# Kernel optimization log

Hardware: AMD Instinct MI355X
Metric: run time of the kernel (lower is better)

## Reference

```python
import jax, jax.numpy as jnp
import numpy as np

N_NODES = 100_000
N_EDGES = 1_250_000
N_GRAPHS = 2048


def gcn_conv(x, src, dst, norm, W, b, n):
    # PyG GCNConv: x' = D^-1/2 (A+I) D^-1/2 (x W) + b  (self-loops already in src/dst)
    h = x @ W                                   # [N, 64]
    msg = h[src] * norm[:, None]                # [E+N, 64] gather + scale
    out = jax.ops.segment_sum(msg, dst, num_segments=n)  # scatter-add
    return out + b


def build_norm(edge_index, n):
    # add self loops, compute symmetric gcn normalization
    loop = jnp.arange(n, dtype=edge_index.dtype)
    src = jnp.concatenate([edge_index[0], loop])
    dst = jnp.concatenate([edge_index[1], loop])
    deg = jax.ops.segment_sum(jnp.ones_like(dst, dtype=jnp.float32), dst, num_segments=n)
    dinv = jnp.where(deg > 0, jax.lax.rsqrt(deg), 0.0)
    norm = dinv[src] * dinv[dst]
    return src, dst, norm


def setup_inputs() -> dict:
    key = jax.random.key(0)
    ks = jax.random.split(key, 11)
    return {
        "x": jax.random.randint(ks[0], (N_NODES,), 0, 28, dtype=jnp.int32),
        "edge_index": jax.random.randint(ks[1], (2, N_EDGES), 0, N_NODES, dtype=jnp.int32),
        "edge_attr": jax.random.randint(ks[2], (N_EDGES,), 0, 4, dtype=jnp.int32),
        "batch": jnp.sort(jax.random.randint(ks[3], (N_NODES,), 0, N_GRAPHS, dtype=jnp.int32)),
        "emb_table": jax.random.normal(ks[4], (28, 64), dtype=jnp.float32),
        "W1": jax.random.normal(ks[5], (64, 64), dtype=jnp.float32) * 0.125,
        "b1": jax.random.normal(ks[6], (64,), dtype=jnp.float32) * 0.02,
        "W2": jax.random.normal(ks[7], (64, 64), dtype=jnp.float32) * 0.125,
        "b2": jax.random.normal(ks[8], (64,), dtype=jnp.float32) * 0.02,
        "lin_W": jax.random.normal(ks[9], (64, 1), dtype=jnp.float32) * 0.125,
        "lin_b": jax.random.normal(ks[10], (1,), dtype=jnp.float32) * 0.02,
    }


def reference(x, edge_index, edge_attr, batch, emb_table, W1, b1, W2, b2, lin_W, lin_b):
    n = x.shape[0]
    src, dst, norm = build_norm(edge_index, n)
    h = emb_table[x]                                   # node embedding lookup [N, 64]
    h = jax.nn.relu(gcn_conv(h, src, dst, norm, W1, b1, n))
    # dropout is identity at inference (training=False)
    emb = gcn_conv(h, src, dst, norm, W2, b2, n)        # [N, 64]
    y = emb @ lin_W + lin_b                              # [N, 1]
    out = jax.ops.segment_sum(y, batch, num_segments=N_GRAPHS)  # graph readout
    return out.squeeze(-1)                               # [N_GRAPHS]
```

## Files before the change

### kernel.cpp

```cpp
#include <hip/hip_runtime.h>

#define N_CLS 28
#define DIM   64
#define VB    128
#define VB_SH 7
#define SLK   32
#define NBKT_S 800
#define PT_T  512
#define IPT   12
#define PTILE (PT_T * IPT)
#define STG   9280

__global__ void __launch_bounds__(PT_T)
k_part(const int* __restrict__ src, const int* __restrict__ dst,
       int* __restrict__ ebkt,
       const float* __restrict__ emb, const float* __restrict__ W1,
       const float* __restrict__ W2, const float* __restrict__ linW,
       const float* __restrict__ b2, const float* __restrict__ linb,
       float* __restrict__ T1g, float* __restrict__ ug, float* __restrict__ ccg,
       float* __restrict__ out,
       int E, int nbkt, int nblk, int out_size) {
    int tid = threadIdx.x, b = blockIdx.x;
    if (b == nblk) {
        int lane = tid & 63, wv = tid >> 6;
        for (int r = wv; r < N_CLS; r += PT_T / 64) {
            float acc = 0.f;
#pragma unroll
            for (int k = 0; k < DIM; ++k) acc += emb[r * DIM + k] * W1[k * DIM + lane];
            T1g[r * DIM + lane] = acc;
        }
        if (wv == 0) {
            float acc = 0.f;
#pragma unroll
            for (int k = 0; k < DIM; ++k) acc += W2[lane * DIM + k] * linW[k];
            ug[lane] = acc;
        }
        if (tid == 0) {
            float s = 0.f;
            for (int k = 0; k < DIM; ++k) s += b2[k] * linW[k];
            ccg[0] = s + linb[0];
        }
        for (int i = tid; i < out_size; i += PT_T) out[i] = 0.f;
        return;
    }
    __shared__ int h[NBKT_S];
    __shared__ int offs[NBKT_S];
    __shared__ int sc[1024];
    __shared__ __align__(16) int stage[STG];
    for (int i = tid; i < nbkt; i += PT_T) h[i] = 0;
    __syncthreads();
    int s0 = b * PTILE;
    int pk[IPT], ar[IPT];
#pragma unroll
    for (int g = 0; g < IPT / 4; ++g) {
        int i4 = s0 + (g * PT_T + tid) * 4;
        if (i4 + 3 < E) {
            int4 sv = *(const int4*)&src[i4];
            int4 dv = *(const int4*)&dst[i4];
            int ss[4] = {sv.x, sv.y, sv.z, sv.w};
            int dd[4] = {dv.x, dv.y, dv.z, dv.w};
#pragma unroll
            for (int j = 0; j < 4; ++j) {
                int bkt = dd[j] >> VB_SH;
                int r = atomicAdd(&h[bkt], 1);
                pk[g * 4 + j] = ss[j] | ((dd[j] & (VB - 1)) << 17);
                ar[g * 4 + j] = bkt | (r << 10);
            }
        } else {
#pragma unroll
            for (int j = 0; j < 4; ++j) {
                int idx = i4 + j;
                ar[g * 4 + j] = -1;
                if (idx < E) {
                    int s = src[idx], d = dst[idx];
                    int bkt = d >> VB_SH;
                    int r = atomicAdd(&h[bkt], 1);
                    pk[g * 4 + j] = s | ((d & (VB - 1)) << 17);
                    ar[g * 4 + j] = bkt | (r << 10);
                }
            }
        }
    }
    __syncthreads();
    int w0 = (tid < nbkt) ? ((min(h[tid], SLK - 1) + 4) & ~3) : 0;
    int w1 = (tid + 512 < nbkt) ? ((min(h[tid + 512], SLK - 1) + 4) & ~3) : 0;
    sc[tid] = w0; sc[tid + 512] = w1;
    __syncthreads();
    for (int o = 1; o < 1024; o <<= 1) {
        int a0 = (tid >= o) ? sc[tid - o] : 0;
        int a1 = (tid + 512 >= o) ? sc[tid + 512 - o] : 0;
        __syncthreads();
        sc[tid] += a0; sc[tid + 512] += a1;
        __syncthreads();
    }
    if (tid < nbkt) offs[tid] = sc[tid] - w0;
    if (tid + 512 < nbkt) offs[tid + 512] = sc[tid + 512] - w1;
    __syncthreads();
    for (int i = tid; i < nbkt; i += PT_T) stage[offs[i]] = min(h[i], SLK - 1);
#pragma unroll
    for (int k = 0; k < IPT; ++k) {
        int a = ar[k];
        if (a >= 0) {
            int bkt = a & 1023, r = a >> 10;
            if (r < SLK - 1) stage[offs[bkt] + 1 + r] = pk[k];
        }
    }
    __syncthreads();
    for (int i = tid; i < nbkt; i += PT_T) {
        int c = min(h[i], SLK - 1);
        int nq = (c + 4) >> 2;
        int4* gq = (int4*)(ebkt + ((size_t)i * nblk + b) * SLK);
        const int4* sq = (const int4*)&stage[offs[i]];
        for (int q = 0; q < nq; ++q) gq[q] = sq[q];
    }
}

#define RUN_FOREACH(rv, BODY)                                            \
    {                                                                    \
        int4 q0 = (rv)[0];                                               \
        int c = q0.x;                                                    \
        int e3[3] = {q0.y, q0.z, q0.w};                                  \
        _Pragma("unroll")                                                \
        for (int j = 0; j < 3; ++j) if (j < c) { int p = e3[j]; BODY; }  \
        for (int base = 3; base < c; base += 4) {                        \
            int4 q = (rv)[(base + 1) >> 2];                              \
            int e4[4] = {q.x, q.y, q.z, q.w};                            \
            _Pragma("unroll")                                            \
            for (int j = 0; j < 4; ++j)                                  \
                if (base + j < c) { int p = e4[j]; BODY; }               \
        }                                                                \
    }

__global__ void __launch_bounds__(256)
k_deg(const int* __restrict__ ebkt, const int* __restrict__ x,
      float2* __restrict__ xd, int N, int nblk) {
    __shared__ int dg[VB];
    int tid = threadIdx.x, k = blockIdx.x;
    if (tid < VB) dg[tid] = 0;
    __syncthreads();
    if (tid < nblk) {
        const int4* rv = (const int4*)(ebkt + ((size_t)k * nblk + tid) * SLK);
        RUN_FOREACH(rv, atomicAdd(&dg[p >> 17], 1));
    }
    __syncthreads();
    int v = k * VB + tid;
    if (tid < VB && v < N)
        xd[v] = make_float2(rsqrtf((float)(dg[tid] + 1)), __int_as_float(x[v]));
}

__global__ void __launch_bounds__(256)
k_l1(const int* __restrict__ ebkt, const float2* __restrict__ xd,
     const float* __restrict__ T1, const float* __restrict__ b1,
     const float* __restrict__ u, float* __restrict__ t, int N, int nblk) {
    __shared__ __align__(16) float cnt[VB * N_CLS];
    __shared__ float T1s[N_CLS * DIM];
    __shared__ float b1s[DIM], us[DIM];
    int tid = threadIdx.x, b = blockIdx.x;
    for (int i = tid; i < VB * N_CLS; i += 256) cnt[i] = 0.f;
    for (int i = tid; i < N_CLS * DIM; i += 256) T1s[i] = T1[i];
    if (tid < DIM) { b1s[tid] = b1[tid]; us[tid] = u[tid]; }
    __syncthreads();
    if (tid < nblk) {
        const int4* rv = (const int4*)(ebkt + ((size_t)b * nblk + tid) * SLK);
        RUN_FOREACH(rv, {
            float2 xs = xd[p & 0x1FFFF];
            atomicAdd(&cnt[(p >> 17) * N_CLS + __float_as_int(xs.y)], xs.x);
        });
    }
    __syncthreads();
    int wave = tid >> 6, lane = tid & 63;
    float tc[N_CLS];
#pragma unroll
    for (int c = 0; c < N_CLS; ++c) tc[c] = T1s[c * DIM + lane];
    int v0 = b * VB;
#pragma unroll 4
    for (int it = 0; it < VB / 4; ++it) {
        int lv = wave * (VB / 4) + it;
        int v = v0 + lv;
        if (v >= N) break;
        float2 pv = xd[v];
        float dv = pv.x;
        int xv = __float_as_int(pv.y);
        const float4* row = (const float4*)&cnt[lv * N_CLS];
        float acc = dv * T1s[xv * DIM + lane];
#pragma unroll
        for (int q4 = 0; q4 < 7; ++q4) {
            float4 r = row[q4];
            acc += r.x * tc[q4 * 4 + 0] + r.y * tc[q4 * 4 + 1]
                 + r.z * tc[q4 * 4 + 2] + r.w * tc[q4 * 4 + 3];
        }
        float hh = fmaxf(dv * acc + b1s[lane], 0.f);
        float q = hh * us[lane];
#pragma unroll
        for (int off = 32; off; off >>= 1) q += __shfl_down(q, off);
        if (lane == 0) t[v] = dv * q;
    }
}

__global__ void __launch_bounds__(256)
k_l2(const int* __restrict__ ebkt, const float2* __restrict__ xd,
     const float* __restrict__ t, const float* __restrict__ cc,
     const int* __restrict__ batch, float* __restrict__ out,
     int N, int n_graphs, int nblk) {
    __shared__ float acc[VB];
    __shared__ float og[64];
    __shared__ int g0s;
    int tid = threadIdx.x, k = blockIdx.x;
    if (tid < VB) acc[tid] = 0.f;
    if (tid < 64) og[tid] = 0.f;
    if (tid == 0) g0s = batch[min(k * VB, N - 1)];
    __syncthreads();
    if (tid < nblk) {
        const int4* rv = (const int4*)(ebkt + ((size_t)k * nblk + tid) * SLK);
        RUN_FOREACH(rv, atomicAdd(&acc[p >> 17], t[p & 0x1FFFF]));
    }
    __syncthreads();
    int v = k * VB + tid;
    if (tid < VB && v < N) {
        float y = xd[v].x * (acc[tid] + t[v]) + cc[0];
        int g = batch[v];
        int off = g - g0s;
        if (off < 64) atomicAdd(&og[off], y);
        else atomicAdd(&out[g], y);
    }
    __syncthreads();
    if (tid < 64) {
        float val = og[tid];
        int g = g0s + tid;
        if (val != 0.f && g < n_graphs) atomicAdd(&out[g], val);
    }
}

extern "C" void kernel_launch(void* const* d_in, const int* in_sizes, int n_in,
                              void* d_out, int out_size, void* d_ws, size_t ws_size,
                              hipStream_t stream) {
    const int*   x     = (const int*)d_in[0];
    const int*   ei    = (const int*)d_in[1];
    const int*   batch = (const int*)d_in[3];
    const float* emb   = (const float*)d_in[4];
    const float* W1    = (const float*)d_in[5];
    const float* b1    = (const float*)d_in[6];
    const float* W2    = (const float*)d_in[7];
    const float* b2    = (const float*)d_in[8];
    const float* linW  = (const float*)d_in[9];
    const float* linb  = (const float*)d_in[10];

    const int N = in_sizes[0];
    const int E = in_sizes[1] / 2;
    const int* srcp = ei;
    const int* dstp = ei + E;
    float* out = (float*)d_out;

    const int nbkt = (N + VB - 1) >> VB_SH;
    const int nblk = (E + PTILE - 1) / PTILE;

    char* w = (char*)d_ws;
    float2* xd   = (float2*)w; w += (size_t)N * 8;
    float*  t    = (float*)w;  w += (size_t)N * 4;
    int*    ebkt = (int*)w;    w += (size_t)nbkt * nblk * SLK * 4;
    float*  T1   = (float*)w;  w += (size_t)N_CLS * DIM * 4;
    float*  u    = (float*)w;  w += DIM * 4;
    float*  cc   = (float*)w;  w += 16;

    k_part<<<nblk + 1, PT_T, 0, stream>>>(srcp, dstp, ebkt,
                                          emb, W1, W2, linW, b2, linb,
                                          T1, u, cc, out, E, nbkt, nblk, out_size);
    k_deg <<<nbkt, 256, 0, stream>>>(ebkt, x, xd, N, nblk);
    k_l1  <<<nbkt, 256, 0, stream>>>(ebkt, xd, T1, b1, u, t, N, nblk);
    k_l2  <<<nbkt, 256, 0, stream>>>(ebkt, xd, t, cc, batch, out, N, out_size, nblk);
}
```

Before: 70.55 us.

## Split bucket runs across thread pairs, use wave-level scans and DPP reductions

The three consumer kernels now launch 512 threads per block, and each run of bucketed edges is processed by two threads that take alternating elements, halving the serial per-thread chain. The partition kernel replaces its 1024-element block-wide Hillis-Steele scan in shared memory with shuffle-based wave scans plus a small per-wave total array, which cuts down on barriers. In k_l1 the 64-lane reduction uses DPP row operations instead of shuffles, and the result is written from lane 63. The extra threads raise register and occupancy pressure in k_l1, and both threads of a pair still read the same run data.

```diff
diff --git a/kernel.cpp b/kernel.cpp
--- a/kernel.cpp
+++ b/kernel.cpp
@@ -45,7 +45,8 @@
     }
     __shared__ int h[NBKT_S];
     __shared__ int offs[NBKT_S];
-    __shared__ int sc[1024];
+    __shared__ int wt[8];
+    __shared__ int seg0tot;
     __shared__ __align__(16) int stage[STG];
     for (int i = tid; i < nbkt; i += PT_T) h[i] = 0;
     __syncthreads();
@@ -82,20 +83,41 @@
         }
     }
     __syncthreads();
-    int w0 = (tid < nbkt) ? ((min(h[tid], SLK - 1) + 4) & ~3) : 0;
-    int w1 = (tid + 512 < nbkt) ? ((min(h[tid + 512], SLK - 1) + 4) & ~3) : 0;
-    sc[tid] = w0; sc[tid + 512] = w1;
-    __syncthreads();
-    for (int o = 1; o < 1024; o <<= 1) {
-        int a0 = (tid >= o) ? sc[tid - o] : 0;
-        int a1 = (tid + 512 >= o) ? sc[tid + 512 - o] : 0;
+    int lane = tid & 63, wave = tid >> 6;
+    {
+        int w0 = (tid < nbkt) ? ((min(h[tid], SLK - 1) + 4) & ~3) : 0;
+        int incl = w0;
+#pragma unroll
+        for (int o = 1; o < 64; o <<= 1) {
+            int n = __shfl_up(incl, o);
+            if (lane >= o) incl += n;
+        }
+        if (lane == 63) wt[wave] = incl;
         __syncthreads();
-        sc[tid] += a0; sc[tid + 512] += a1;
+        int woff = 0, tot = 0;
+#pragma unroll
+        for (int w2 = 0; w2 < 8; ++w2) { int t2 = wt[w2]; woff += (w2 < wave) ? t2 : 0; tot += t2; }
+        if (tid < nbkt) offs[tid] = woff + incl - w0;
+        if (tid == 0) seg0tot = tot;
         __syncthreads();
     }
-    if (tid < nbkt) offs[tid] = sc[tid] - w0;
-    if (tid + 512 < nbkt) offs[tid + 512] = sc[tid + 512] - w1;
-    __syncthreads();
+    {
+        int i1 = tid + 512;
+        int w1 = (i1 < nbkt) ? ((min(h[i1], SLK - 1) + 4) & ~3) : 0;
+        int incl = w1;
+#pragma unroll
+        for (int o = 1; o < 64; o <<= 1) {
+            int n = __shfl_up(incl, o);
+            if (lane >= o) incl += n;
+        }
+        if (lane == 63) wt[wave] = incl;
+        __syncthreads();
+        int woff = 0;
+#pragma unroll
+        for (int w2 = 0; w2 < 8; ++w2) woff += (w2 < wave) ? wt[w2] : 0;
+        if (i1 < nbkt) offs[i1] = seg0tot + woff + incl - w1;
+        __syncthreads();
+    }
     for (int i = tid; i < nbkt; i += PT_T) stage[offs[i]] = min(h[i], SLK - 1);
 #pragma unroll
     for (int k = 0; k < IPT; ++k) {
@@ -115,32 +137,45 @@
     }
 }
 
-#define RUN_FOREACH(rv, BODY)                                            \
+#define RUN_FOREACH_J(rv, jj, BODY)                                      \
     {                                                                    \
         int4 q0 = (rv)[0];                                               \
         int c = q0.x;                                                    \
         int e3[3] = {q0.y, q0.z, q0.w};                                  \
         _Pragma("unroll")                                                \
-        for (int j = 0; j < 3; ++j) if (j < c) { int p = e3[j]; BODY; }  \
+        for (int j_ = 0; j_ < 3; ++j_)                                   \
+            if (j_ < c && (j_ & 1) == (jj)) { int p = e3[j_]; BODY; }    \
         for (int base = 3; base < c; base += 4) {                        \
             int4 q = (rv)[(base + 1) >> 2];                              \
             int e4[4] = {q.x, q.y, q.z, q.w};                            \
             _Pragma("unroll")                                            \
-            for (int j = 0; j < 4; ++j)                                  \
-                if (base + j < c) { int p = e4[j]; BODY; }               \
+            for (int j_ = 0; j_ < 4; ++j_)                               \
+                if (base + j_ < c && ((base + j_) & 1) == (jj))          \
+                    { int p = e4[j_]; BODY; }                            \
         }                                                                \
     }
 
-__global__ void __launch_bounds__(256)
+__device__ __forceinline__ float wsum64(float q) {
+    q += __int_as_float(__builtin_amdgcn_update_dpp(0, __float_as_int(q), 0x111, 0xf, 0xf, true));
+    q += __int_as_float(__builtin_amdgcn_update_dpp(0, __float_as_int(q), 0x112, 0xf, 0xf, true));
+    q += __int_as_float(__builtin_amdgcn_update_dpp(0, __float_as_int(q), 0x114, 0xf, 0xf, true));
+    q += __int_as_float(__builtin_amdgcn_update_dpp(0, __float_as_int(q), 0x118, 0xf, 0xf, true));
+    q += __int_as_float(__builtin_amdgcn_update_dpp(0, __float_as_int(q), 0x142, 0xa, 0xf, false));
+    q += __int_as_float(__builtin_amdgcn_update_dpp(0, __float_as_int(q), 0x143, 0xc, 0xf, false));
+    return q;
+}
+
+__global__ void __launch_bounds__(512)
 k_deg(const int* __restrict__ ebkt, const int* __restrict__ x,
       float2* __restrict__ xd, int N, int nblk) {
     __shared__ int dg[VB];
     int tid = threadIdx.x, k = blockIdx.x;
     if (tid < VB) dg[tid] = 0;
     __syncthreads();
-    if (tid < nblk) {
-        const int4* rv = (const int4*)(ebkt + ((size_t)k * nblk + tid) * SLK);
-        RUN_FOREACH(rv, atomicAdd(&dg[p >> 17], 1));
+    int rid = tid >> 1, j = tid & 1;
+    if (rid < nblk) {
+        const int4* rv = (const int4*)(ebkt + ((size_t)k * nblk + rid) * SLK);
+        RUN_FOREACH_J(rv, j, atomicAdd(&dg[p >> 17], 1));
     }
     __syncthreads();
     int v = k * VB + tid;
@@ -148,7 +183,7 @@
         xd[v] = make_float2(rsqrtf((float)(dg[tid] + 1)), __int_as_float(x[v]));
 }
 
-__global__ void __launch_bounds__(256)
+__global__ void __launch_bounds__(512)
 k_l1(const int* __restrict__ ebkt, const float2* __restrict__ xd,
      const float* __restrict__ T1, const float* __restrict__ b1,
      const float* __restrict__ u, float* __restrict__ t, int N, int nblk) {
@@ -156,13 +191,14 @@
     __shared__ float T1s[N_CLS * DIM];
     __shared__ float b1s[DIM], us[DIM];
     int tid = threadIdx.x, b = blockIdx.x;
-    for (int i = tid; i < VB * N_CLS; i += 256) cnt[i] = 0.f;
-    for (int i = tid; i < N_CLS * DIM; i += 256) T1s[i] = T1[i];
+    for (int i = tid; i < VB * N_CLS; i += 512) cnt[i] = 0.f;
+    for (int i = tid; i < N_CLS * DIM; i += 512) T1s[i] = T1[i];
     if (tid < DIM) { b1s[tid] = b1[tid]; us[tid] = u[tid]; }
     __syncthreads();
-    if (tid < nblk) {
-        const int4* rv = (const int4*)(ebkt + ((size_t)b * nblk + tid) * SLK);
-        RUN_FOREACH(rv, {
+    int rid = tid >> 1, j = tid & 1;
+    if (rid < nblk) {
+        const int4* rv = (const int4*)(ebkt + ((size_t)b * nblk + rid) * SLK);
+        RUN_FOREACH_J(rv, j, {
             float2 xs = xd[p & 0x1FFFF];
             atomicAdd(&cnt[(p >> 17) * N_CLS + __float_as_int(xs.y)], xs.x);
         });
@@ -172,10 +208,10 @@
     float tc[N_CLS];
 #pragma unroll
     for (int c = 0; c < N_CLS; ++c) tc[c] = T1s[c * DIM + lane];
+    float b1l = b1s[lane], ul = us[lane];
     int v0 = b * VB;
-#pragma unroll 4
-    for (int it = 0; it < VB / 4; ++it) {
-        int lv = wave * (VB / 4) + it;
+    for (int it = 0; it < 16; ++it) {
+        int lv = wave * 16 + it;
         int v = v0 + lv;
         if (v >= N) break;
         float2 pv = xd[v];
@@ -189,15 +225,13 @@
             acc += r.x * tc[q4 * 4 + 0] + r.y * tc[q4 * 4 + 1]
                  + r.z * tc[q4 * 4 + 2] + r.w * tc[q4 * 4 + 3];
         }
-        float hh = fmaxf(dv * acc + b1s[lane], 0.f);
-        float q = hh * us[lane];
-#pragma unroll
-        for (int off = 32; off; off >>= 1) q += __shfl_down(q, off);
-        if (lane == 0) t[v] = dv * q;
-    }
-}
-
-__global__ void __launch_bounds__(256)
+        float hh = fmaxf(dv * acc + b1l, 0.f);
+        float q = wsum64(hh * ul);
+        if (lane == 63) t[v] = dv * q;
+    }
+}
+
+__global__ void __launch_bounds__(512)
 k_l2(const int* __restrict__ ebkt, const float2* __restrict__ xd,
      const float* __restrict__ t, const float* __restrict__ cc,
      const int* __restrict__ batch, float* __restrict__ out,
@@ -210,9 +244,10 @@
     if (tid < 64) og[tid] = 0.f;
     if (tid == 0) g0s = batch[min(k * VB, N - 1)];
     __syncthreads();
-    if (tid < nblk) {
-        const int4* rv = (const int4*)(ebkt + ((size_t)k * nblk + tid) * SLK);
-        RUN_FOREACH(rv, atomicAdd(&acc[p >> 17], t[p & 0x1FFFF]));
+    int rid = tid >> 1, j = tid & 1;
+    if (rid < nblk) {
+        const int4* rv = (const int4*)(ebkt + ((size_t)k * nblk + rid) * SLK);
+        RUN_FOREACH_J(rv, j, atomicAdd(&acc[p >> 17], t[p & 0x1FFFF]));
     }
     __syncthreads();
     int v = k * VB + tid;
@@ -265,7 +300,7 @@
     k_part<<<nblk + 1, PT_T, 0, stream>>>(srcp, dstp, ebkt,
                                           emb, W1, W2, linW, b2, linb,
                                           T1, u, cc, out, E, nbkt, nblk, out_size);
-    k_deg <<<nbkt, 256, 0, stream>>>(ebkt, x, xd, N, nblk);
-    k_l1  <<<nbkt, 256, 0, stream>>>(ebkt, xd, T1, b1, u, t, N, nblk);
-    k_l2  <<<nbkt, 256, 0, stream>>>(ebkt, xd, t, cc, batch, out, N, out_size, nblk);
-}
+    k_deg <<<nbkt, 512, 0, stream>>>(ebkt, x, xd, N, nblk);
+    k_l1  <<<nbkt, 512, 0, stream>>>(ebkt, xd, T1, b1, u, t, N, nblk);
+    k_l2  <<<nbkt, 512, 0, stream>>>(ebkt, xd, t, cc, batch, out, N, out_size, nblk);
+}
```

New measurement: 62.92 us (median of 2 runs). 1.12x faster.
